# Optimization experiments

Measured on AMD Instinct MI355X. Metric: run time of the kernel, lower is better.

Reference implementation:

```python
import jax, jax.numpy as jnp
import numpy as np

S, B, E, H = 2048, 4, 1024, 16
D = E // H  # head_dim = 64


def setup_inputs() -> dict:
    key = jax.random.key(0)
    k1, k2, k3 = jax.random.split(key, 3)
    # xavier-uniform-ish init scales
    query = jax.random.normal(k1, (S, B, E), dtype=jnp.float32)
    in_proj_weight = jax.random.normal(k2, (3 * E, E), dtype=jnp.float32) * (2.0 / (4 * E)) ** 0.5
    in_proj_bias = jnp.zeros((3 * E,), dtype=jnp.float32)
    out_proj_weight = jax.random.normal(k3, (E, E), dtype=jnp.float32) * (1.0 / E) ** 0.5
    out_proj_bias = jnp.zeros((E,), dtype=jnp.float32)
    return {
        "query": query,
        "in_proj_weight": in_proj_weight,
        "in_proj_bias": in_proj_bias,
        "out_proj_weight": out_proj_weight,
        "out_proj_bias": out_proj_bias,
    }


def reference(query, in_proj_weight, in_proj_bias, out_proj_weight, out_proj_bias):
    # Self-attention path (qkv_same): fused in_proj then chunk into q,k,v.
    # query: (S, B, E); F.linear(x, W, b) = x @ W.T + b
    qkv = jnp.einsum('sbe,fe->sbf', query, in_proj_weight) + in_proj_bias  # (S, B, 3E)
    q, k, v = jnp.split(qkv, 3, axis=-1)  # each (S, B, E)
    scaling = D ** (-0.5)
    q = q * scaling
    # reshape to (B*H, S, D): view(S, B*H, D).transpose(0,1)
    def to_bh(x):
        return x.reshape(S, B * H, D).transpose(1, 0, 2)
    q, k, v = to_bh(q), to_bh(k), to_bh(v)
    # scores: (B*H, S, S)
    scores = jnp.einsum('nqd,nkd->nqk', q, k)
    attn = jax.nn.softmax(scores, axis=-1)  # dropout p=0 (inference)
    out = jnp.einsum('nqk,nkd->nqd', attn, v)  # (B*H, S, D)
    out = out.transpose(1, 0, 2).reshape(S, B, E)
    out = jnp.einsum('sbe,fe->sbf', out, out_proj_weight) + out_proj_bias
    return out
```

## Files before the change

kernel.cpp:

```cpp
#include <hip/hip_runtime.h>
#include <hip/hip_bf16.h>


typedef __attribute__((ext_vector_type(8))) short bf16x8;
typedef __attribute__((ext_vector_type(4))) float floatx4;
typedef __attribute__((ext_vector_type(16))) float floatx16;
typedef __attribute__((ext_vector_type(4))) unsigned int uintx4;

#define S_LEN 2048
#define EMB   1024
#define DHEAD 64

static __device__ __forceinline__ unsigned short f2bf(float x) {
    return __builtin_bit_cast(unsigned short, __float2bfloat16(x));
}

static __device__ __forceinline__ unsigned pack_bf16(float a, float b) {
    return (unsigned)f2bf(a) | ((unsigned)f2bf(b) << 16);
}

static __device__ __forceinline__ void dma16(const void* g, void* l) {
    __builtin_amdgcn_global_load_lds(
        (const __attribute__((address_space(1))) unsigned int*)(unsigned long long)g,
        (__attribute__((address_space(3))) unsigned int*)(unsigned int)(unsigned long long)l,
        16, 0, 0);
}

__global__ void detect_kernel(const unsigned short* __restrict__ q, int* __restrict__ flag) {
    __shared__ int cnt;
    if (threadIdx.x == 0) cnt = 0;
    __syncthreads();
    int local = 0;
    for (int i = threadIdx.x; i < 4096; i += 256) {
        unsigned short u = q[i];
        int e = (u >> 7) & 0xFF;
        if (e >= 132) local++;
    }
    atomicAdd(&cnt, local);
    __syncthreads();
    if (threadIdx.x == 0) *flag = (cnt > 100) ? 1 : 0;
}

__global__ void convert_all_kernel(
    const void* __restrict__ s0, const void* __restrict__ s1, const void* __restrict__ s2,
    const void* __restrict__ s3, const void* __restrict__ s4,
    __hip_bfloat16* __restrict__ d0, __hip_bfloat16* __restrict__ d1, __hip_bfloat16* __restrict__ d2,
    __hip_bfloat16* __restrict__ d3, __hip_bfloat16* __restrict__ d4,
    const int* __restrict__ flag)
{
    const int mode = *flag;
    const int c0 = 2097152, c1 = c0 + 786432, c2 = c1 + 768, c3 = c2 + 262144, c4 = c3 + 256;
    int i = blockIdx.x * blockDim.x + threadIdx.x;
    const int stride = gridDim.x * blockDim.x;
    for (; i < c4; i += stride) {
        const void* s; __hip_bfloat16* d; int off;
        if (i < c0)      { s = s0; d = d0; off = i; }
        else if (i < c1) { s = s1; d = d1; off = i - c0; }
        else if (i < c2) { s = s2; d = d2; off = i - c1; }
        else if (i < c3) { s = s3; d = d3; off = i - c2; }
        else             { s = s4; d = d4; off = i - c3; }
        if (mode) {
            float4 v = ((const float4*)s)[off];
            ushort4 o;
            o.x = f2bf(v.x); o.y = f2bf(v.y); o.z = f2bf(v.z); o.w = f2bf(v.w);
            ((ushort4*)d)[off] = o;
        } else {
            ((ushort4*)d)[off] = ((const ushort4*)s)[off];
        }
    }
}

#define GEMM_STAGE(As, Bs, Aptr, Bptr, ldA, ldB)                                       \
    {                                                                                  \
        const int srow = (l >> 3);                                                     \
        const int cG   = ((l & 7) ^ srow) * 8;                                         \
        _Pragma("unroll")                                                              \
        for (int j = 0; j < 4; j++) {                                                  \
            const int r0 = wave * 32 + j * 8;                                          \
            dma16(Aptr + (size_t)(r0 + srow) * ldA + cG, &As[r0][0]);                  \
            dma16(Bptr + (size_t)(r0 + srow) * ldB + cG, &Bs[r0][0]);                  \
        }                                                                              \
    }

__global__ __launch_bounds__(256) void qkv_gemm_kernel(
    const __hip_bfloat16* __restrict__ X,
    const __hip_bfloat16* __restrict__ W,
    const __hip_bfloat16* __restrict__ bias,
    __hip_bfloat16* __restrict__ Qws,
    __hip_bfloat16* __restrict__ Kws,
    __hip_bfloat16* __restrict__ Vws)
{
    __shared__ alignas(16) __hip_bfloat16 As[128][64];
    __shared__ alignas(16) __hip_bfloat16 Bs[128][64];

    const int t    = threadIdx.x;
    const int l    = t & 63;
    const int wave = t >> 6;
    const int l15  = l & 15;
    const int quad = l >> 4;
    const int wr   = (wave >> 1) * 64;
    const int wc   = (wave & 1) * 64;
    const int rowBase = blockIdx.x * 128;
    const int colBase = blockIdx.y * 128;

    floatx4 acc[4][4] = {};

    for (int k0 = 0; k0 < EMB; k0 += 64) {
        __syncthreads();
        const __hip_bfloat16* Ap = X + (size_t)rowBase * EMB + k0;
        const __hip_bfloat16* Bp = W + (size_t)colBase * EMB + k0;
        GEMM_STAGE(As, Bs, Ap, Bp, EMB, EMB)
        __syncthreads();
#pragma unroll
        for (int ks = 0; ks < 2; ks++) {
            bf16x8 af[4], bfr[4];
#pragma unroll
            for (int ti = 0; ti < 4; ti++) {
                const int rA = wr + ti * 16 + l15;
                af[ti] = *(const bf16x8*)(&As[rA][(((ks * 4 + quad) ^ (rA & 7)) * 8)]);
            }
#pragma unroll
            for (int tj = 0; tj < 4; tj++) {
                const int rB = wc + tj * 16 + l15;
                bfr[tj] = *(const bf16x8*)(&Bs[rB][(((ks * 4 + quad) ^ (rB & 7)) * 8)]);
            }
#pragma unroll
            for (int ti = 0; ti < 4; ti++)
#pragma unroll
                for (int tj = 0; tj < 4; tj++)
                    acc[ti][tj] = __builtin_amdgcn_mfma_f32_16x16x32_bf16(
                        af[ti], bfr[tj], acc[ti][tj], 0, 0, 0);
        }
    }

    const float QSCALE = 0.125f * 1.44269504088896f;
#pragma unroll
    for (int tj = 0; tj < 4; tj++) {
        const int col = colBase + wc + tj * 16 + l15;
        const int sec = col >> 10;
        const int e   = col & 1023;
        const int h   = e >> 6;
        const int d   = e & 63;
        const float bv = __bfloat162float(bias[col]);
#pragma unroll
        for (int ti = 0; ti < 4; ti++) {
#pragma unroll
            for (int r = 0; r < 4; r++) {
                const int row = rowBase + wr + ti * 16 + quad * 4 + r;
                const int s  = row >> 2;
                const int b  = row & 3;
                const int nh = b * 16 + h;
                const float val = acc[ti][tj][r] + bv;
                if (sec == 0) {
                    Qws[((size_t)nh * S_LEN + s) * DHEAD + d] = __float2bfloat16(val * QSCALE);
                } else if (sec == 1) {
                    Kws[((size_t)nh * S_LEN + s) * DHEAD + d] = __float2bfloat16(val);
                } else {
                    Vws[((size_t)nh * DHEAD + d) * S_LEN + s] = __float2bfloat16(val);
                }
            }
        }
    }
}

__global__ __launch_bounds__(256, 2) void attn_kernel(
    const __hip_bfloat16* __restrict__ Qws,
    const __hip_bfloat16* __restrict__ Kws,
    const __hip_bfloat16* __restrict__ Vws,
    __hip_bfloat16* __restrict__ AOut)
{
    __shared__ alignas(16) __hip_bfloat16 Ks[2][64][64];
    __shared__ alignas(16) __hip_bfloat16 Vts[2][64][64];

    const int n  = blockIdx.x;
    const int q0 = blockIdx.y * 256;
    const int t    = threadIdx.x;
    const int l    = t & 63;
    const int wave = t >> 6;
    const int l31  = l & 31;
    const int hi   = l >> 5;

    const int srow = (l >> 3);
    const int cG   = ((l & 7) ^ srow) * 8;

#pragma unroll
    for (int j = 0; j < 2; j++) {
        const int r0 = wave * 16 + j * 8;
        dma16(Kws + ((size_t)n * S_LEN + r0 + srow) * DHEAD + cG, &Ks[0][r0][0]);
        dma16(Vws + ((size_t)n * DHEAD + r0 + srow) * S_LEN + cG, &Vts[0][r0][0]);
    }

    bf16x8 qb[2][4];
#pragma unroll
    for (int qt = 0; qt < 2; qt++)
#pragma unroll
        for (int ds = 0; ds < 4; ds++)
            qb[qt][ds] = *(const bf16x8*)(Qws +
                ((size_t)n * S_LEN + q0 + wave * 64 + qt * 32 + l31) * DHEAD + ds * 16 + hi * 8);

    floatx16 o[2][2] = {};
    float lsum[2] = {};

    int cur = 0;
    for (int kt = 0; kt < 32; kt++) {
        __syncthreads();

        if (kt < 31) {
            const int key0 = (kt + 1) * 64;
#pragma unroll
            for (int j = 0; j < 2; j++) {
                const int r0 = wave * 16 + j * 8;
                dma16(Kws + ((size_t)n * S_LEN + key0 + r0 + srow) * DHEAD + cG, &Ks[cur ^ 1][r0][0]);
                dma16(Vws + ((size_t)n * DHEAD + r0 + srow) * S_LEN + key0 + cG, &Vts[cur ^ 1][r0][0]);
            }
        }

        bf16x8 kb[2][4];
#pragma unroll
        for (int kt2 = 0; kt2 < 2; kt2++)
#pragma unroll
            for (int ds = 0; ds < 4; ds++) {
                const int key = kt2 * 32 + l31;
                kb[kt2][ds] = *(const bf16x8*)(&Ks[cur][key][(((ds * 2 + hi) ^ (key & 7)) * 8)]);
            }

        bf16x8 pa[2][4];
#pragma unroll
        for (int qt = 0; qt < 2; qt++) {
            floatx16 sacc[2] = {};
            __builtin_amdgcn_s_setprio(1);
#pragma unroll
            for (int ds = 0; ds < 4; ds++)
#pragma unroll
                for (int kt2 = 0; kt2 < 2; kt2++)
                    sacc[kt2] = __builtin_amdgcn_mfma_f32_32x32x16_bf16(
                        kb[kt2][ds], qb[qt][ds], sacc[kt2], 0, 0, 0);
            __builtin_amdgcn_s_setprio(0);

#pragma unroll
            for (int kt2 = 0; kt2 < 2; kt2++) {
                float pv[16];
#pragma unroll
                for (int r = 0; r < 16; r++)
                    pv[r] = __builtin_amdgcn_exp2f(sacc[kt2][r]);
                lsum[qt] += (((pv[0] + pv[1]) + (pv[2] + pv[3])) + ((pv[4] + pv[5]) + (pv[6] + pv[7])))
                          + (((pv[8] + pv[9]) + (pv[10] + pv[11])) + ((pv[12] + pv[13]) + (pv[14] + pv[15])));
#pragma unroll
                for (int sl = 0; sl < 2; sl++) {
                    const int b = sl * 8;
                    unsigned lo01 = pack_bf16(pv[b + 0], pv[b + 1]);
                    unsigned lo23 = pack_bf16(pv[b + 2], pv[b + 3]);
                    unsigned hi01 = pack_bf16(pv[b + 4], pv[b + 5]);
                    unsigned hi23 = pack_bf16(pv[b + 6], pv[b + 7]);
                    unsigned p_lo01 = __shfl_xor(lo01, 32);
                    unsigned p_lo23 = __shfl_xor(lo23, 32);
                    unsigned p_hi01 = __shfl_xor(hi01, 32);
                    unsigned p_hi23 = __shfl_xor(hi23, 32);
                    uintx4 w;
                    w[0] = hi ? p_hi01 : lo01;
                    w[1] = hi ? p_hi23 : lo23;
                    w[2] = hi ? hi01 : p_lo01;
                    w[3] = hi ? hi23 : p_lo23;
                    pa[qt][kt2 * 2 + sl] = __builtin_bit_cast(bf16x8, w);
                }
            }
        }

        bf16x8 va[2][4];
#pragma unroll
        for (int dt = 0; dt < 2; dt++)
#pragma unroll
            for (int kslab = 0; kslab < 4; kslab++) {
                const int d = dt * 32 + l31;
                va[dt][kslab] = *(const bf16x8*)(&Vts[cur][d][(((kslab * 2 + hi) ^ (d & 7)) * 8)]);
            }

        __builtin_amdgcn_s_setprio(1);
#pragma unroll
        for (int kslab = 0; kslab < 4; kslab++)
#pragma unroll
            for (int dt = 0; dt < 2; dt++)
#pragma unroll
                for (int qt = 0; qt < 2; qt++)
                    o[dt][qt] = __builtin_amdgcn_mfma_f32_32x32x16_bf16(
                        va[dt][kslab], pa[qt][kslab], o[dt][qt], 0, 0, 0);
        __builtin_amdgcn_s_setprio(0);

        cur ^= 1;
    }

    const int bb  = n >> 4;
    const int h64 = (n & 15) * 64;
#pragma unroll
    for (int qt = 0; qt < 2; qt++) {
        const float denom = lsum[qt] + __shfl_xor(lsum[qt], 32);
        const float linv = 1.0f / denom;
        const int q = q0 + wave * 64 + qt * 32 + l31;
#pragma unroll
        for (int dt = 0; dt < 2; dt++) {
#pragma unroll
            for (int g = 0; g < 4; g++) {
                const int d = dt * 32 + g * 8 + hi * 4;
                ushort4 w;
                w.x = f2bf(o[dt][qt][4 * g + 0] * linv);
                w.y = f2bf(o[dt][qt][4 * g + 1] * linv);
                w.z = f2bf(o[dt][qt][4 * g + 2] * linv);
                w.w = f2bf(o[dt][qt][4 * g + 3] * linv);
                *(ushort4*)(AOut + ((size_t)q * 4 + bb) * EMB + h64 + d) = w;
            }
        }
    }
}

__global__ __launch_bounds__(256) void out_gemm_kernel(
    const __hip_bfloat16* __restrict__ A,
    const __hip_bfloat16* __restrict__ W,
    const __hip_bfloat16* __restrict__ bias,
    void* __restrict__ out,
    const int* __restrict__ flag)
{
    __shared__ alignas(16) __hip_bfloat16 As[128][64];
    __shared__ alignas(16) __hip_bfloat16 Bs[128][64];

    const int t    = threadIdx.x;
    const int l    = t & 63;
    const int wave = t >> 6;
    const int l15  = l & 15;
    const int quad = l >> 4;
    const int wr   = (wave >> 1) * 64;
    const int wc   = (wave & 1) * 64;
    const int rowBase = blockIdx.x * 128;
    const int colBase = blockIdx.y * 128;
    const int mode = *flag;

    floatx4 acc[4][4] = {};

    for (int k0 = 0; k0 < EMB; k0 += 64) {
        __syncthreads();
        const __hip_bfloat16* Ap = A + (size_t)rowBase * EMB + k0;
        const __hip_bfloat16* Bp = W + (size_t)colBase * EMB + k0;
        GEMM_STAGE(As, Bs, Ap, Bp, EMB, EMB)
        __syncthreads();
#pragma unroll
        for (int ks = 0; ks < 2; ks++) {
            bf16x8 af[4], bfr[4];
#pragma unroll
            for (int ti = 0; ti < 4; ti++) {
                const int rA = wr + ti * 16 + l15;
                af[ti] = *(const bf16x8*)(&As[rA][(((ks * 4 + quad) ^ (rA & 7)) * 8)]);
            }
#pragma unroll
            for (int tj = 0; tj < 4; tj++) {
                const int rB = wc + tj * 16 + l15;
                bfr[tj] = *(const bf16x8*)(&Bs[rB][(((ks * 4 + quad) ^ (rB & 7)) * 8)]);
            }
#pragma unroll
            for (int ti = 0; ti < 4; ti++)
#pragma unroll
                for (int tj = 0; tj < 4; tj++)
                    acc[ti][tj] = __builtin_amdgcn_mfma_f32_16x16x32_bf16(
                        af[ti], bfr[tj], acc[ti][tj], 0, 0, 0);
        }
    }

#pragma unroll
    for (int tj = 0; tj < 4; tj++) {
        const int col = colBase + wc + tj * 16 + l15;
        const float bv = __bfloat162float(bias[col]);
#pragma unroll
        for (int ti = 0; ti < 4; ti++) {
#pragma unroll
            for (int r = 0; r < 4; r++) {
                const int row = rowBase + wr + ti * 16 + quad * 4 + r;
                const float val = acc[ti][tj][r] + bv;
                if (mode) {
                    ((float*)out)[(size_t)row * EMB + col] = val;
                } else {
                    ((__hip_bfloat16*)out)[(size_t)row * EMB + col] = __float2bfloat16(val);
                }
            }
        }
    }
}

extern "C" void kernel_launch(void* const* d_in, const int* in_sizes, int n_in,
                              void* d_out, int out_size, void* d_ws, size_t ws_size,
                              hipStream_t stream) {
    const void* query = d_in[0];
    const void* w_in  = d_in[1];
    const void* b_in  = d_in[2];
    const void* w_out = d_in[3];
    const void* b_out = d_in[4];

    char* ws = (char*)d_ws;
    int*            flag   = (int*)ws;
    __hip_bfloat16* Xc     = (__hip_bfloat16*)(ws + 256);
    __hip_bfloat16* Winc   = Xc   + (size_t)8192 * 1024;
    __hip_bfloat16* binc   = Winc + (size_t)3072 * 1024;
    __hip_bfloat16* Woutc  = binc + 3072;
    __hip_bfloat16* boutc  = Woutc + (size_t)1024 * 1024;
    __hip_bfloat16* Qws    = boutc + 1024;
    __hip_bfloat16* Kws    = Qws + (size_t)8388608;
    __hip_bfloat16* Vws    = Kws + (size_t)8388608;
    __hip_bfloat16* AOut   = Vws + (size_t)8388608;

    detect_kernel<<<1, 256, 0, stream>>>((const unsigned short*)query, flag);

    convert_all_kernel<<<2048, 256, 0, stream>>>(query, w_in, b_in, w_out, b_out,
                                                 Xc, Winc, binc, Woutc, boutc, flag);

    qkv_gemm_kernel<<<dim3(64, 24), 256, 0, stream>>>(Xc, Winc, binc, Qws, Kws, Vws);
    attn_kernel<<<dim3(64, 8), 256, 0, stream>>>(Qws, Kws, Vws, AOut);
    out_gemm_kernel<<<dim3(64, 8), 256, 0, stream>>>(AOut, Woutc, boutc, d_out, flag);
}
```

Measured before the change: 317.9 us.

## Load K and V fragments directly from global memory, dropping LDS staging

The attention kernel no longer stages K and V tiles in double-buffered shared memory with async DMA and per-iteration barriers. Each wave now loads its K and V MFMA fragments straight from global memory into registers. This removes the LDS traffic and __syncthreads, but each of the four waves fetches the same K/V data separately, so the kernel relies on L1/L2 for reuse. The loads are also not prefetched ahead of the compute.

```diff
diff --git a/kernel.cpp b/kernel.cpp
--- a/kernel.cpp
+++ b/kernel.cpp
@@ -169,9 +169,6 @@
     const __hip_bfloat16* __restrict__ Vws,
     __hip_bfloat16* __restrict__ AOut)
 {
-    __shared__ alignas(16) __hip_bfloat16 Ks[2][64][64];
-    __shared__ alignas(16) __hip_bfloat16 Vts[2][64][64];
-
     const int n  = blockIdx.x;
     const int q0 = blockIdx.y * 256;
     const int t    = threadIdx.x;
@@ -180,16 +177,6 @@
     const int l31  = l & 31;
     const int hi   = l >> 5;
 
-    const int srow = (l >> 3);
-    const int cG   = ((l & 7) ^ srow) * 8;
-
-#pragma unroll
-    for (int j = 0; j < 2; j++) {
-        const int r0 = wave * 16 + j * 8;
-        dma16(Kws + ((size_t)n * S_LEN + r0 + srow) * DHEAD + cG, &Ks[0][r0][0]);
-        dma16(Vws + ((size_t)n * DHEAD + r0 + srow) * S_LEN + cG, &Vts[0][r0][0]);
-    }
-
     bf16x8 qb[2][4];
 #pragma unroll
     for (int qt = 0; qt < 2; qt++)
@@ -198,31 +185,30 @@
             qb[qt][ds] = *(const bf16x8*)(Qws +
                 ((size_t)n * S_LEN + q0 + wave * 64 + qt * 32 + l31) * DHEAD + ds * 16 + hi * 8);
 
+    const __hip_bfloat16* Kn = Kws + (size_t)n * S_LEN * DHEAD;
+    const __hip_bfloat16* Vn = Vws + (size_t)n * DHEAD * S_LEN;
+
     floatx16 o[2][2] = {};
     float lsum[2] = {};
 
-    int cur = 0;
     for (int kt = 0; kt < 32; kt++) {
-        __syncthreads();
-
-        if (kt < 31) {
-            const int key0 = (kt + 1) * 64;
-#pragma unroll
-            for (int j = 0; j < 2; j++) {
-                const int r0 = wave * 16 + j * 8;
-                dma16(Kws + ((size_t)n * S_LEN + key0 + r0 + srow) * DHEAD + cG, &Ks[cur ^ 1][r0][0]);
-                dma16(Vws + ((size_t)n * DHEAD + r0 + srow) * S_LEN + key0 + cG, &Vts[cur ^ 1][r0][0]);
-            }
-        }
+        const int key0 = kt * 64;
 
         bf16x8 kb[2][4];
 #pragma unroll
         for (int kt2 = 0; kt2 < 2; kt2++)
 #pragma unroll
-            for (int ds = 0; ds < 4; ds++) {
-                const int key = kt2 * 32 + l31;
-                kb[kt2][ds] = *(const bf16x8*)(&Ks[cur][key][(((ds * 2 + hi) ^ (key & 7)) * 8)]);
-            }
+            for (int ds = 0; ds < 4; ds++)
+                kb[kt2][ds] = *(const bf16x8*)(Kn +
+                    (size_t)(key0 + kt2 * 32 + l31) * DHEAD + ds * 16 + hi * 8);
+
+        bf16x8 va[2][4];
+#pragma unroll
+        for (int dt = 0; dt < 2; dt++)
+#pragma unroll
+            for (int kslab = 0; kslab < 4; kslab++)
+                va[dt][kslab] = *(const bf16x8*)(Vn +
+                    (size_t)(dt * 32 + l31) * S_LEN + key0 + kslab * 16 + hi * 8);
 
         bf16x8 pa[2][4];
 #pragma unroll
@@ -266,15 +252,6 @@
             }
         }
 
-        bf16x8 va[2][4];
-#pragma unroll
-        for (int dt = 0; dt < 2; dt++)
-#pragma unroll
-            for (int kslab = 0; kslab < 4; kslab++) {
-                const int d = dt * 32 + l31;
-                va[dt][kslab] = *(const bf16x8*)(&Vts[cur][d][(((kslab * 2 + hi) ^ (d & 7)) * 8)]);
-            }
-
         __builtin_amdgcn_s_setprio(1);
 #pragma unroll
         for (int kslab = 0; kslab < 4; kslab++)
@@ -285,8 +262,6 @@
                     o[dt][qt] = __builtin_amdgcn_mfma_f32_32x32x16_bf16(
                         va[dt][kslab], pa[qt][kslab], o[dt][qt], 0, 0, 0);
         __builtin_amdgcn_s_setprio(0);
-
-        cur ^= 1;
     }
 
     const int bb  = n >> 4;
```

After: 353.0 us. +11.0%, slower.
